# Optimization experiments

Hardware: AMD Instinct MI355X
Metric: run time of the kernel (lower is better)

The kernel has to match this reference:

```python
import jax, jax.numpy as jnp
import numpy as np

L, H, FF, NH = 6, 1024, 4096, 8
HD = H // NH
B, S = 4, 1024
EPS = 1e-5


def _fp8_roundtrip(w):
    # matches torch path: cast to float8_e4m3fn and back (done once at init, no grad)
    return w.astype(jnp.float8_e4m3fn).astype(w.dtype)


def setup_inputs() -> dict:
    key = jax.random.key(0)
    ks = jax.random.split(key, 6)
    x = jax.random.normal(ks[0], (B, S, H), dtype=jnp.float32)
    sH = 1.0 / np.sqrt(H)
    sF = 1.0 / np.sqrt(FF)
    qkv_w = _fp8_roundtrip(jax.random.normal(ks[1], (L, 3 * H, H), jnp.float32) * sH)
    proj_w = _fp8_roundtrip(jax.random.normal(ks[2], (L, H, H), jnp.float32) * sH)
    fc1_w = _fp8_roundtrip(jax.random.normal(ks[3], (L, FF, H), jnp.float32) * sH)
    fc2_w = _fp8_roundtrip(jax.random.normal(ks[4], (L, H, FF), jnp.float32) * sF)
    return {
        "x": x,
        "qkv_w": qkv_w, "qkv_b": jnp.zeros((L, 3 * H), jnp.float32),
        "proj_w": proj_w, "proj_b": jnp.zeros((L, H), jnp.float32),
        "fc1_w": fc1_w, "fc1_b": jnp.zeros((L, FF), jnp.float32),
        "fc2_w": fc2_w, "fc2_b": jnp.zeros((L, H), jnp.float32),
        "ln1_s": jnp.ones((L, H), jnp.float32), "ln1_b": jnp.zeros((L, H), jnp.float32),
        "ln2_s": jnp.ones((L, H), jnp.float32), "ln2_b": jnp.zeros((L, H), jnp.float32),
    }


def _layernorm(x, scale, bias):
    mu = jnp.mean(x, axis=-1, keepdims=True)
    var = jnp.var(x, axis=-1, keepdims=True)
    return (x - mu) / jnp.sqrt(var + EPS) * scale + bias


def reference(x, qkv_w, qkv_b, proj_w, proj_b, fc1_w, fc1_b, fc2_w, fc2_b,
              ln1_s, ln1_b, ln2_s, ln2_b):
    b, s, h = x.shape
    for i in range(L):
        # --- attention block ---
        residual = x
        hx = _layernorm(x, ln1_s[i], ln1_b[i])
        qkv = hx @ qkv_w[i].T + qkv_b[i]                       # [b, s, 3h]
        q, k, v = jnp.split(qkv, 3, axis=-1)
        q = q.reshape(b, s, NH, HD).transpose(0, 2, 1, 3)      # [b, nh, s, hd]
        k = k.reshape(b, s, NH, HD).transpose(0, 2, 1, 3)
        v = v.reshape(b, s, NH, HD).transpose(0, 2, 1, 3)
        scores = jnp.einsum('bhqd,bhkd->bhqk', q, k) / np.sqrt(HD)
        attn = jax.nn.softmax(scores, axis=-1)
        out = jnp.einsum('bhqk,bhkd->bhqd', attn, v)           # [b, nh, s, hd]
        out = out.transpose(0, 2, 1, 3).reshape(b, s, h)
        x = out @ proj_w[i].T + proj_b[i] + residual
        # --- FFN block ---
        residual = x
        hx = _layernorm(x, ln2_s[i], ln2_b[i])
        ff = jax.nn.relu(hx @ fc1_w[i].T + fc1_b[i])
        x = ff @ fc2_w[i].T + fc2_b[i] + residual
    return x
```

## Files before the change

### kernel.cpp

```cpp
#include <hip/hip_runtime.h>
#include <stdint.h>

typedef __bf16 bf16;
typedef __bf16 bf16x4 __attribute__((ext_vector_type(4)));
typedef __bf16 bf16x8 __attribute__((ext_vector_type(8)));
typedef float  f32x4  __attribute__((ext_vector_type(4)));

#define NLAYER 6
#define HDIM   1024
#define FFDIM  4096
#define NHEAD  8
#define HEADD  128
#define SEQ    1024
#define NTOK   4096

__device__ __forceinline__ void g2l16(const void* g, void* l) {
  __builtin_amdgcn_global_load_lds(
      (const __attribute__((address_space(1))) void*)g,
      (__attribute__((address_space(3))) void*)l, 16, 0, 0);
}

__global__ __launch_bounds__(256) void cvt_w(const float* __restrict__ in,
                                             bf16* __restrict__ out, int n8) {
  int i = blockIdx.x * 256 + threadIdx.x;
  if (i >= n8) return;
  const f32x4* p = (const f32x4*)in + (size_t)i * 2;
  f32x4 a = p[0], b = p[1];
  bf16x8 o;
  o[0] = (bf16)a[0]; o[1] = (bf16)a[1]; o[2] = (bf16)a[2]; o[3] = (bf16)a[3];
  o[4] = (bf16)b[0]; o[5] = (bf16)b[1]; o[6] = (bf16)b[2]; o[7] = (bf16)b[3];
  *((bf16x8*)out + i) = o;
}

__global__ __launch_bounds__(256) void ln_k(const float* __restrict__ x,
                                            const float* __restrict__ sc,
                                            const float* __restrict__ bi,
                                            bf16* __restrict__ out) {
  int row = blockIdx.x, t = threadIdx.x;
  f32x4 v = *((const f32x4*)(x + (size_t)row * HDIM) + t);
  float s = v[0] + v[1] + v[2] + v[3];
  float q = v[0]*v[0] + v[1]*v[1] + v[2]*v[2] + v[3]*v[3];
#pragma unroll
  for (int m = 1; m < 64; m <<= 1) {
    s += __shfl_xor(s, m, 64);
    q += __shfl_xor(q, m, 64);
  }
  __shared__ float ss[4], qq[4];
  if ((t & 63) == 0) { ss[t >> 6] = s; qq[t >> 6] = q; }
  __syncthreads();
  s = ss[0] + ss[1] + ss[2] + ss[3];
  q = qq[0] + qq[1] + qq[2] + qq[3];
  float mu  = s * (1.f / HDIM);
  float var = q * (1.f / HDIM) - mu * mu;
  float rs  = rsqrtf(var + 1e-5f);
  f32x4 g = *((const f32x4*)sc + t);
  f32x4 b = *((const f32x4*)bi + t);
  bf16x4 o;
#pragma unroll
  for (int j = 0; j < 4; j++) o[j] = (bf16)((v[j] - mu) * rs * g[j] + b[j]);
  *((bf16x4*)(out + (size_t)row * HDIM) + t) = o;
}

template <bool RELU, bool RESID, bool OUTF32, bool SPLITV>
__global__ __launch_bounds__(256) void gemm_bt(const bf16* __restrict__ A,
                                               const bf16* __restrict__ W,
                                               const float* __restrict__ bias,
                                               const float* resid, void* outp,
                                               bf16* __restrict__ vt,
                                               int M, int N, int K) {
  constexpr int BK = 64;
  __shared__ bf16 As[128 * BK];
  __shared__ bf16 Bs[128 * BK];
  int tid = threadIdx.x;
  int lane = tid & 63, w = tid >> 6;
  int g = lane >> 4, r = lane & 15;
  int wr = w >> 1, wc = w & 1;
  int nbx = N >> 7;
  int bm = blockIdx.x / nbx, bn = blockIdx.x % nbx;
  const bf16* Ab = A + (size_t)bm * 128 * K;
  const bf16* Wb = W + (size_t)bn * 128 * K;
  f32x4 acc[4][4] = {};

  for (int k0 = 0; k0 < K; k0 += BK) {
#pragma unroll
    for (int i = 0; i < 4; ++i) {
      int cb = i * 256 + w * 64;
      int c  = cb + lane;
      int row = c >> 3;
      int kk  = ((c & 7) ^ (row & 7)) << 3;
      g2l16(Ab + (size_t)row * K + k0 + kk, (char*)As + cb * 16);
      g2l16(Wb + (size_t)row * K + k0 + kk, (char*)Bs + cb * 16);
    }
    __syncthreads();
#pragma unroll
    for (int ks = 0; ks < 2; ++ks) {
      bf16x8 af[4], bfr[4];
#pragma unroll
      for (int mi = 0; mi < 4; mi++) {
        int row = wr * 64 + mi * 16 + r;
        af[mi] = *(const bf16x8*)((const char*)As + row * 128 +
                                  ((ks * 64 + g * 16) ^ ((row & 7) << 4)));
      }
#pragma unroll
      for (int ni = 0; ni < 4; ni++) {
        int row = wc * 64 + ni * 16 + r;
        bfr[ni] = *(const bf16x8*)((const char*)Bs + row * 128 +
                                   ((ks * 64 + g * 16) ^ ((row & 7) << 4)));
      }
#pragma unroll
      for (int mi = 0; mi < 4; mi++)
#pragma unroll
        for (int ni = 0; ni < 4; ni++)
          acc[mi][ni] = __builtin_amdgcn_mfma_f32_16x16x32_bf16(
              af[mi], bfr[ni], acc[mi][ni], 0, 0, 0);
    }
    __syncthreads();
  }

#pragma unroll
  for (int ni = 0; ni < 4; ++ni) {
    int col = bn * 128 + wc * 64 + ni * 16 + r;
    float bv = bias[col];
    bool vpart = SPLITV && (bn * 128 + wc * 64 + ni * 16) >= 2048;
    if (vpart) {
      int hh = (col - 2048) >> 7, dd = col & 127;
#pragma unroll
      for (int mi = 0; mi < 4; ++mi) {
        int row0 = bm * 128 + wr * 64 + mi * 16 + g * 4;
        int bb = row0 >> 10, ss = row0 & 1023;
        bf16x4 o;
#pragma unroll
        for (int j = 0; j < 4; j++) o[j] = (bf16)(acc[mi][ni][j] + bv);
        *(bf16x4*)(vt + ((size_t)((bb * NHEAD + hh) * HEADD + dd)) * SEQ + ss) = o;
      }
    } else {
#pragma unroll
      for (int mi = 0; mi < 4; ++mi) {
        int row0 = bm * 128 + wr * 64 + mi * 16 + g * 4;
#pragma unroll
        for (int j = 0; j < 4; j++) {
          size_t idx = (size_t)(row0 + j) * N + col;
          float v = acc[mi][ni][j] + bv;
          if constexpr (RELU) v = fmaxf(v, 0.f);
          if constexpr (RESID) v += resid[idx];
          if constexpr (OUTF32) ((float*)outp)[idx] = v;
          else                  ((bf16*)outp)[idx] = (bf16)v;
        }
      }
    }
  }
}

__global__ __launch_bounds__(256) void attn_k(const bf16* __restrict__ qkv,
                                              const bf16* __restrict__ vt,
                                              bf16* __restrict__ out) {
  __shared__ bf16 Ks[64 * 128];
  __shared__ bf16 VT[128 * 64];
  __shared__ bf16 Ps[4][1024];
  int qt = blockIdx.x, h = blockIdx.y, b = blockIdx.z;
  int tid = threadIdx.x, lane = tid & 63, w = tid >> 6;
  int g = lane >> 4, r = lane & 15;
  int q0 = qt * 64;
  size_t tok0 = (size_t)b * SEQ;
  char* psw = (char*)Ps + w * 2048;

  bf16x8 qf[4];
  {
    const bf16* qp = qkv + (tok0 + q0 + w * 16 + r) * 3072 + h * HEADD;
#pragma unroll
    for (int ks = 0; ks < 4; ks++) qf[ks] = *(const bf16x8*)(qp + ks * 32 + g * 8);
  }
  f32x4 oacc[8] = {};
  float mprev[4], lsum[4];
#pragma unroll
  for (int j = 0; j < 4; j++) { mprev[j] = -1e30f; lsum[j] = 0.f; }
  const float scl = 0.08838834764831845f;
  const bf16* vtb = vt + (size_t)(b * NHEAD + h) * HEADD * SEQ;

  for (int c0 = 0; c0 < SEQ; c0 += 64) {
    const bf16* kbase = qkv + (tok0 + c0) * 3072 + 1024 + h * HEADD;
#pragma unroll
    for (int i = 0; i < 4; i++) {
      int cb = i * 256 + w * 64;
      int c  = cb + lane;
      int krow = c >> 4;
      int kkk  = ((c & 15) ^ (krow & 7)) << 3;
      g2l16(kbase + (size_t)krow * 3072 + kkk, (char*)Ks + cb * 16);
      int vrow = c >> 3;
      int vcol = ((c & 7) ^ (vrow & 7)) << 3;
      g2l16(vtb + (size_t)vrow * SEQ + c0 + vcol, (char*)VT + cb * 16);
    }
    __syncthreads();

    f32x4 sacc[4] = {};
#pragma unroll
    for (int ks = 0; ks < 4; ks++) {
#pragma unroll
      for (int cb = 0; cb < 4; cb++) {
        int row = cb * 16 + r;
        bf16x8 kf = *(const bf16x8*)((const char*)Ks + row * 256 +
                                     ((ks * 64 + g * 16) ^ ((row & 7) << 4)));
        sacc[cb] = __builtin_amdgcn_mfma_f32_16x16x32_bf16(qf[ks], kf, sacc[cb], 0, 0, 0);
      }
    }
#pragma unroll
    for (int cb = 0; cb < 4; cb++) {
      sacc[cb][0] *= scl; sacc[cb][1] *= scl; sacc[cb][2] *= scl; sacc[cb][3] *= scl;
    }
    float sf[4];
#pragma unroll
    for (int j = 0; j < 4; j++) {
      float m = fmaxf(fmaxf(sacc[0][j], sacc[1][j]), fmaxf(sacc[2][j], sacc[3][j]));
      m = fmaxf(m, __shfl_xor(m, 1, 64));
      m = fmaxf(m, __shfl_xor(m, 2, 64));
      m = fmaxf(m, __shfl_xor(m, 4, 64));
      m = fmaxf(m, __shfl_xor(m, 8, 64));
      float mn = fmaxf(mprev[j], m);
      float f  = __expf(mprev[j] - mn);
      mprev[j] = mn; sf[j] = f;
      float rs = 0.f;
#pragma unroll
      for (int cb = 0; cb < 4; cb++) {
        float p = __expf(sacc[cb][j] - mn);
        sacc[cb][j] = p; rs += p;
      }
      rs += __shfl_xor(rs, 1, 64);
      rs += __shfl_xor(rs, 2, 64);
      rs += __shfl_xor(rs, 4, 64);
      rs += __shfl_xor(rs, 8, 64);
      lsum[j] = lsum[j] * f + rs;
    }
#pragma unroll
    for (int nb = 0; nb < 8; nb++) {
      oacc[nb][0] *= sf[0]; oacc[nb][1] *= sf[1];
      oacc[nb][2] *= sf[2]; oacc[nb][3] *= sf[3];
    }
#pragma unroll
    for (int cb = 0; cb < 4; cb++) {
      int cbyte = cb * 32 + r * 2;
#pragma unroll
      for (int j = 0; j < 4; j++) {
        int q = g * 4 + j;
        *(bf16*)(psw + q * 128 + (cbyte ^ ((q & 7) << 4))) = (bf16)sacc[cb][j];
      }
    }
    asm volatile("s_waitcnt lgkmcnt(0)" ::: "memory");
    __builtin_amdgcn_sched_barrier(0);
#pragma unroll
    for (int cs = 0; cs < 2; cs++) {
      bf16x8 pf = *(const bf16x8*)(psw + r * 128 + ((cs * 64 + g * 16) ^ ((r & 7) << 4)));
#pragma unroll
      for (int nb = 0; nb < 8; nb++) {
        int vrow = nb * 16 + r;
        bf16x8 vf = *(const bf16x8*)((const char*)VT + vrow * 128 +
                                     ((cs * 64 + g * 16) ^ ((vrow & 7) << 4)));
        oacc[nb] = __builtin_amdgcn_mfma_f32_16x16x32_bf16(pf, vf, oacc[nb], 0, 0, 0);
      }
    }
    __syncthreads();
  }

  float rl[4];
#pragma unroll
  for (int j = 0; j < 4; j++) rl[j] = 1.f / lsum[j];
#pragma unroll
  for (int nb = 0; nb < 8; nb++)
#pragma unroll
    for (int j = 0; j < 4; j++)
      out[(tok0 + q0 + w * 16 + g * 4 + j) * HDIM + h * HEADD + nb * 16 + r] =
          (bf16)(oacc[nb][j] * rl[j]);
}

extern "C" void kernel_launch(void* const* d_in, const int* in_sizes, int n_in,
                              void* d_out, int out_size, void* d_ws, size_t ws_size,
                              hipStream_t stream) {
  const float* x_in   = (const float*)d_in[0];
  const float* qkv_w  = (const float*)d_in[1];
  const float* qkv_b  = (const float*)d_in[2];
  const float* proj_w = (const float*)d_in[3];
  const float* proj_b = (const float*)d_in[4];
  const float* fc1_w  = (const float*)d_in[5];
  const float* fc1_b  = (const float*)d_in[6];
  const float* fc2_w  = (const float*)d_in[7];
  const float* fc2_b  = (const float*)d_in[8];
  const float* ln1_s  = (const float*)d_in[9];
  const float* ln1_b  = (const float*)d_in[10];
  const float* ln2_s  = (const float*)d_in[11];
  const float* ln2_b  = (const float*)d_in[12];

  char* ws = (char*)d_ws;
  size_t o = 0;
  bf16* Wq = (bf16*)(ws + o); o += (size_t)NLAYER * 3 * HDIM * HDIM * 2;
  bf16* Wp = (bf16*)(ws + o); o += (size_t)NLAYER * HDIM * HDIM * 2;
  bf16* W1 = (bf16*)(ws + o); o += (size_t)NLAYER * FFDIM * HDIM * 2;
  bf16* W2 = (bf16*)(ws + o); o += (size_t)NLAYER * HDIM * FFDIM * 2;
  bf16* hx   = (bf16*)(ws + o); o += (size_t)NTOK * HDIM * 2;
  bf16* qkvb = (bf16*)(ws + o); o += (size_t)NTOK * 3 * HDIM * 2;
  bf16* Vt   = (bf16*)(ws + o); o += (size_t)NTOK * HDIM * 2;
  bf16* aout = (bf16*)(ws + o); o += (size_t)NTOK * HDIM * 2;
  bf16* ffb  = (bf16*)(ws + o); o += (size_t)NTOK * FFDIM * 2;
  float* xbuf = (float*)d_out;

  {
    int n8;
    n8 = NLAYER * 3 * HDIM * HDIM / 8;
    cvt_w<<<(n8 + 255) / 256, 256, 0, stream>>>(qkv_w, Wq, n8);
    n8 = NLAYER * HDIM * HDIM / 8;
    cvt_w<<<(n8 + 255) / 256, 256, 0, stream>>>(proj_w, Wp, n8);
    n8 = NLAYER * FFDIM * HDIM / 8;
    cvt_w<<<(n8 + 255) / 256, 256, 0, stream>>>(fc1_w, W1, n8);
    n8 = NLAYER * HDIM * FFDIM / 8;
    cvt_w<<<(n8 + 255) / 256, 256, 0, stream>>>(fc2_w, W2, n8);
  }

  for (int i = 0; i < NLAYER; i++) {
    const float* xc = (i == 0) ? x_in : xbuf;
    ln_k<<<NTOK, 256, 0, stream>>>(xc, ln1_s + i * HDIM, ln1_b + i * HDIM, hx);
    gemm_bt<false, false, false, true><<<(NTOK / 128) * (3 * HDIM / 128), 256, 0, stream>>>(
        hx, Wq + (size_t)i * 3 * HDIM * HDIM, qkv_b + i * 3 * HDIM, nullptr,
        qkvb, Vt, NTOK, 3 * HDIM, HDIM);
    attn_k<<<dim3(SEQ / 64, NHEAD, 4), 256, 0, stream>>>(qkvb, Vt, aout);
    gemm_bt<false, true, true, false><<<(NTOK / 128) * (HDIM / 128), 256, 0, stream>>>(
        aout, Wp + (size_t)i * HDIM * HDIM, proj_b + i * HDIM, xc,
        xbuf, nullptr, NTOK, HDIM, HDIM);
    ln_k<<<NTOK, 256, 0, stream>>>(xbuf, ln2_s + i * HDIM, ln2_b + i * HDIM, hx);
    gemm_bt<true, false, false, false><<<(NTOK / 128) * (FFDIM / 128), 256, 0, stream>>>(
        hx, W1 + (size_t)i * FFDIM * HDIM, fc1_b + i * FFDIM, nullptr,
        ffb, nullptr, NTOK, FFDIM, HDIM);
    gemm_bt<false, true, true, false><<<(NTOK / 128) * (HDIM / 128), 256, 0, stream>>>(
        ffb, W2 + (size_t)i * HDIM * FFDIM, fc2_b + i * HDIM, xbuf,
        xbuf, nullptr, NTOK, HDIM, FFDIM);
  }
  (void)in_sizes; (void)n_in; (void)out_size; (void)ws_size;
}
```

Measured before the change: 1.761 ms.

## Double-buffer GEMM LDS tiles with 8 waves and XCD-aware block swizzle

```diff
diff --git a/kernel.cpp b/kernel.cpp
--- a/kernel.cpp
+++ b/kernel.cpp
@@ -62,66 +62,80 @@
 }
 
 template <bool RELU, bool RESID, bool OUTF32, bool SPLITV>
-__global__ __launch_bounds__(256) void gemm_bt(const bf16* __restrict__ A,
-                                               const bf16* __restrict__ W,
-                                               const float* __restrict__ bias,
-                                               const float* resid, void* outp,
-                                               bf16* __restrict__ vt,
-                                               int M, int N, int K) {
-  constexpr int BK = 64;
-  __shared__ bf16 As[128 * BK];
-  __shared__ bf16 Bs[128 * BK];
+__global__ __launch_bounds__(512) void gemm8(const bf16* __restrict__ A,
+                                             const bf16* __restrict__ W,
+                                             const float* __restrict__ bias,
+                                             const float* resid, void* outp,
+                                             bf16* __restrict__ vt,
+                                             int M, int N, int K) {
+  __shared__ bf16 As[2][128 * 64];
+  __shared__ bf16 Bs[2][128 * 64];
   int tid = threadIdx.x;
   int lane = tid & 63, w = tid >> 6;
   int g = lane >> 4, r = lane & 15;
-  int wr = w >> 1, wc = w & 1;
+  int wr = w >> 2, wc = w & 3;
   int nbx = N >> 7;
-  int bm = blockIdx.x / nbx, bn = blockIdx.x % nbx;
+  int cpx = gridDim.x >> 3;
+  int swz = (blockIdx.x & 7) * cpx + (blockIdx.x >> 3);
+  int bm = swz / nbx, bn = swz % nbx;
   const bf16* Ab = A + (size_t)bm * 128 * K;
   const bf16* Wb = W + (size_t)bn * 128 * K;
-  f32x4 acc[4][4] = {};
-
-  for (int k0 = 0; k0 < K; k0 += BK) {
-#pragma unroll
-    for (int i = 0; i < 4; ++i) {
-      int cb = i * 256 + w * 64;
-      int c  = cb + lane;
+  f32x4 acc[4][2] = {};
+
+  auto STAGE = [&](int buf, int k0) {
+#pragma unroll
+    for (int i = 0; i < 2; ++i) {
+      int c = i * 512 + tid;
       int row = c >> 3;
-      int kk  = ((c & 7) ^ (row & 7)) << 3;
-      g2l16(Ab + (size_t)row * K + k0 + kk, (char*)As + cb * 16);
-      g2l16(Wb + (size_t)row * K + k0 + kk, (char*)Bs + cb * 16);
-    }
-    __syncthreads();
+      int kk = ((c & 7) ^ (row & 7)) << 3;
+      g2l16(Ab + (size_t)row * K + k0 + kk, (char*)As[buf] + c * 16);
+      g2l16(Wb + (size_t)row * K + k0 + kk, (char*)Bs[buf] + c * 16);
+    }
+  };
+  auto COMPUTE = [&](int buf) {
 #pragma unroll
     for (int ks = 0; ks < 2; ++ks) {
-      bf16x8 af[4], bfr[4];
+      bf16x8 af[4], bfr[2];
 #pragma unroll
       for (int mi = 0; mi < 4; mi++) {
         int row = wr * 64 + mi * 16 + r;
-        af[mi] = *(const bf16x8*)((const char*)As + row * 128 +
+        af[mi] = *(const bf16x8*)((const char*)As[buf] + row * 128 +
                                   ((ks * 64 + g * 16) ^ ((row & 7) << 4)));
       }
 #pragma unroll
-      for (int ni = 0; ni < 4; ni++) {
-        int row = wc * 64 + ni * 16 + r;
-        bfr[ni] = *(const bf16x8*)((const char*)Bs + row * 128 +
+      for (int ni = 0; ni < 2; ni++) {
+        int row = wc * 32 + ni * 16 + r;
+        bfr[ni] = *(const bf16x8*)((const char*)Bs[buf] + row * 128 +
                                    ((ks * 64 + g * 16) ^ ((row & 7) << 4)));
       }
+      __builtin_amdgcn_s_setprio(1);
 #pragma unroll
       for (int mi = 0; mi < 4; mi++)
 #pragma unroll
-        for (int ni = 0; ni < 4; ni++)
+        for (int ni = 0; ni < 2; ni++)
           acc[mi][ni] = __builtin_amdgcn_mfma_f32_16x16x32_bf16(
               af[mi], bfr[ni], acc[mi][ni], 0, 0, 0);
-    }
+      __builtin_amdgcn_s_setprio(0);
+    }
+  };
+
+  int nt = K >> 6;
+  STAGE(0, 0);
+  __syncthreads();
+  int cur = 0;
+  for (int t = 0; t < nt - 1; ++t) {
+    STAGE(cur ^ 1, (t + 1) << 6);
+    COMPUTE(cur);
     __syncthreads();
-  }
-
-#pragma unroll
-  for (int ni = 0; ni < 4; ++ni) {
-    int col = bn * 128 + wc * 64 + ni * 16 + r;
+    cur ^= 1;
+  }
+  COMPUTE(cur);
+
+#pragma unroll
+  for (int ni = 0; ni < 2; ++ni) {
+    int col = bn * 128 + wc * 32 + ni * 16 + r;
     float bv = bias[col];
-    bool vpart = SPLITV && (bn * 128 + wc * 64 + ni * 16) >= 2048;
+    bool vpart = SPLITV && (bn * 128 + wc * 32 + ni * 16) >= 2048;
     if (vpart) {
       int hh = (col - 2048) >> 7, dd = col & 127;
 #pragma unroll
@@ -316,18 +330,18 @@
   for (int i = 0; i < NLAYER; i++) {
     const float* xc = (i == 0) ? x_in : xbuf;
     ln_k<<<NTOK, 256, 0, stream>>>(xc, ln1_s + i * HDIM, ln1_b + i * HDIM, hx);
-    gemm_bt<false, false, false, true><<<(NTOK / 128) * (3 * HDIM / 128), 256, 0, stream>>>(
+    gemm8<false, false, false, true><<<(NTOK / 128) * (3 * HDIM / 128), 512, 0, stream>>>(
         hx, Wq + (size_t)i * 3 * HDIM * HDIM, qkv_b + i * 3 * HDIM, nullptr,
         qkvb, Vt, NTOK, 3 * HDIM, HDIM);
     attn_k<<<dim3(SEQ / 64, NHEAD, 4), 256, 0, stream>>>(qkvb, Vt, aout);
-    gemm_bt<false, true, true, false><<<(NTOK / 128) * (HDIM / 128), 256, 0, stream>>>(
+    gemm8<false, true, true, false><<<(NTOK / 128) * (HDIM / 128), 512, 0, stream>>>(
         aout, Wp + (size_t)i * HDIM * HDIM, proj_b + i * HDIM, xc,
         xbuf, nullptr, NTOK, HDIM, HDIM);
     ln_k<<<NTOK, 256, 0, stream>>>(xbuf, ln2_s + i * HDIM, ln2_b + i * HDIM, hx);
-    gemm_bt<true, false, false, false><<<(NTOK / 128) * (FFDIM / 128), 256, 0, stream>>>(
+    gemm8<true, false, false, false><<<(NTOK / 128) * (FFDIM / 128), 512, 0, stream>>>(
         hx, W1 + (size_t)i * FFDIM * HDIM, fc1_b + i * FFDIM, nullptr,
         ffb, nullptr, NTOK, FFDIM, HDIM);
-    gemm_bt<false, true, true, false><<<(NTOK / 128) * (HDIM / 128), 256, 0, stream>>>(
+    gemm8<false, true, true, false><<<(NTOK / 128) * (HDIM / 128), 512, 0, stream>>>(
         ffb, W2 + (size_t)i * HDIM * FFDIM, fc2_b + i * HDIM, xbuf,
         xbuf, nullptr, NTOK, HDIM, FFDIM);
   }
```

Result: faster. 1.567 ms (-11.0%).

## Add 4-stage LDS prefetch pipeline and XCD block swizzle to GEMM

Applied to the files above, without the earlier changes.

```diff
diff --git a/kernel.cpp b/kernel.cpp
--- a/kernel.cpp
+++ b/kernel.cpp
@@ -62,60 +62,88 @@
 }
 
 template <bool RELU, bool RESID, bool OUTF32, bool SPLITV>
-__global__ __launch_bounds__(256) void gemm_bt(const bf16* __restrict__ A,
-                                               const bf16* __restrict__ W,
-                                               const float* __restrict__ bias,
-                                               const float* resid, void* outp,
-                                               bf16* __restrict__ vt,
-                                               int M, int N, int K) {
-  constexpr int BK = 64;
-  __shared__ bf16 As[128 * BK];
-  __shared__ bf16 Bs[128 * BK];
+__global__ __launch_bounds__(256) void gemm4(const bf16* __restrict__ A,
+                                             const bf16* __restrict__ W,
+                                             const float* __restrict__ bias,
+                                             const float* resid, void* outp,
+                                             bf16* __restrict__ vt,
+                                             int M, int N, int K) {
+  __shared__ bf16 As[4][128 * 64];
+  __shared__ bf16 Bs[4][128 * 64];
   int tid = threadIdx.x;
   int lane = tid & 63, w = tid >> 6;
   int g = lane >> 4, r = lane & 15;
   int wr = w >> 1, wc = w & 1;
   int nbx = N >> 7;
-  int bm = blockIdx.x / nbx, bn = blockIdx.x % nbx;
+  int cpx = gridDim.x >> 3;
+  int swz = (blockIdx.x & 7) * cpx + (blockIdx.x >> 3);
+  int bm = swz / nbx, bn = swz % nbx;
   const bf16* Ab = A + (size_t)bm * 128 * K;
   const bf16* Wb = W + (size_t)bn * 128 * K;
   f32x4 acc[4][4] = {};
 
-  for (int k0 = 0; k0 < K; k0 += BK) {
+  auto STAGE = [&](int buf, int k0) {
 #pragma unroll
     for (int i = 0; i < 4; ++i) {
-      int cb = i * 256 + w * 64;
-      int c  = cb + lane;
+      int c = i * 256 + tid;
       int row = c >> 3;
-      int kk  = ((c & 7) ^ (row & 7)) << 3;
-      g2l16(Ab + (size_t)row * K + k0 + kk, (char*)As + cb * 16);
-      g2l16(Wb + (size_t)row * K + k0 + kk, (char*)Bs + cb * 16);
-    }
-    __syncthreads();
+      int kk = ((c & 7) ^ (row & 7)) << 3;
+      g2l16(Ab + (size_t)row * K + k0 + kk, (char*)As[buf] + c * 16);
+      g2l16(Wb + (size_t)row * K + k0 + kk, (char*)Bs[buf] + c * 16);
+    }
+  };
+  auto COMPUTE = [&](int buf) {
 #pragma unroll
     for (int ks = 0; ks < 2; ++ks) {
       bf16x8 af[4], bfr[4];
 #pragma unroll
       for (int mi = 0; mi < 4; mi++) {
         int row = wr * 64 + mi * 16 + r;
-        af[mi] = *(const bf16x8*)((const char*)As + row * 128 +
+        af[mi] = *(const bf16x8*)((const char*)As[buf] + row * 128 +
                                   ((ks * 64 + g * 16) ^ ((row & 7) << 4)));
       }
 #pragma unroll
       for (int ni = 0; ni < 4; ni++) {
         int row = wc * 64 + ni * 16 + r;
-        bfr[ni] = *(const bf16x8*)((const char*)Bs + row * 128 +
+        bfr[ni] = *(const bf16x8*)((const char*)Bs[buf] + row * 128 +
                                    ((ks * 64 + g * 16) ^ ((row & 7) << 4)));
       }
+      __builtin_amdgcn_s_setprio(1);
 #pragma unroll
       for (int mi = 0; mi < 4; mi++)
 #pragma unroll
         for (int ni = 0; ni < 4; ni++)
           acc[mi][ni] = __builtin_amdgcn_mfma_f32_16x16x32_bf16(
               af[mi], bfr[ni], acc[mi][ni], 0, 0, 0);
-    }
-    __syncthreads();
-  }
+      __builtin_amdgcn_s_setprio(0);
+    }
+  };
+
+  int nt = K >> 6;
+  STAGE(0, 0);
+  STAGE(1, 64);
+  STAGE(2, 128);
+  int t = 0;
+  for (; t < nt - 3; ++t) {
+    asm volatile("s_waitcnt vmcnt(16)" ::: "memory");
+    __builtin_amdgcn_s_barrier();
+    __builtin_amdgcn_sched_barrier(0);
+    STAGE((t + 3) & 3, (t + 3) << 6);
+    __builtin_amdgcn_sched_barrier(0);
+    COMPUTE(t & 3);
+  }
+  asm volatile("s_waitcnt vmcnt(16)" ::: "memory");
+  __builtin_amdgcn_s_barrier();
+  __builtin_amdgcn_sched_barrier(0);
+  COMPUTE(t & 3); ++t;
+  asm volatile("s_waitcnt vmcnt(8)" ::: "memory");
+  __builtin_amdgcn_s_barrier();
+  __builtin_amdgcn_sched_barrier(0);
+  COMPUTE(t & 3); ++t;
+  asm volatile("s_waitcnt vmcnt(0)" ::: "memory");
+  __builtin_amdgcn_s_barrier();
+  __builtin_amdgcn_sched_barrier(0);
+  COMPUTE(t & 3);
 
 #pragma unroll
   for (int ni = 0; ni < 4; ++ni) {
@@ -149,6 +177,7 @@
       }
     }
   }
+  (void)M;
 }
 
 __global__ __launch_bounds__(256) void attn_k(const bf16* __restrict__ qkv,
@@ -316,18 +345,18 @@
   for (int i = 0; i < NLAYER; i++) {
     const float* xc = (i == 0) ? x_in : xbuf;
     ln_k<<<NTOK, 256, 0, stream>>>(xc, ln1_s + i * HDIM, ln1_b + i * HDIM, hx);
-    gemm_bt<false, false, false, true><<<(NTOK / 128) * (3 * HDIM / 128), 256, 0, stream>>>(
+    gemm4<false, false, false, true><<<(NTOK / 128) * (3 * HDIM / 128), 256, 0, stream>>>(
         hx, Wq + (size_t)i * 3 * HDIM * HDIM, qkv_b + i * 3 * HDIM, nullptr,
         qkvb, Vt, NTOK, 3 * HDIM, HDIM);
     attn_k<<<dim3(SEQ / 64, NHEAD, 4), 256, 0, stream>>>(qkvb, Vt, aout);
-    gemm_bt<false, true, true, false><<<(NTOK / 128) * (HDIM / 128), 256, 0, stream>>>(
+    gemm4<false, true, true, false><<<(NTOK / 128) * (HDIM / 128), 256, 0, stream>>>(
         aout, Wp + (size_t)i * HDIM * HDIM, proj_b + i * HDIM, xc,
         xbuf, nullptr, NTOK, HDIM, HDIM);
     ln_k<<<NTOK, 256, 0, stream>>>(xbuf, ln2_s + i * HDIM, ln2_b + i * HDIM, hx);
-    gemm_bt<true, false, false, false><<<(NTOK / 128) * (FFDIM / 128), 256, 0, stream>>>(
+    gemm4<true, false, false, false><<<(NTOK / 128) * (FFDIM / 128), 256, 0, stream>>>(
         hx, W1 + (size_t)i * FFDIM * HDIM, fc1_b + i * FFDIM, nullptr,
         ffb, nullptr, NTOK, FFDIM, HDIM);
-    gemm_bt<false, true, true, false><<<(NTOK / 128) * (HDIM / 128), 256, 0, stream>>>(
+    gemm4<false, true, true, false><<<(NTOK / 128) * (HDIM / 128), 256, 0, stream>>>(
         ffb, W2 + (size_t)i * HDIM * FFDIM, fc2_b + i * HDIM, xbuf,
         xbuf, nullptr, NTOK, HDIM, FFDIM);
   }
```

Result: slower. 1.947 ms (+10.6%).

## Split-K the N=1024 GEMMs with atomic accumulation and swizzle block order

Applied to the files above, without the earlier changes.

```diff
diff --git a/kernel.cpp b/kernel.cpp
--- a/kernel.cpp
+++ b/kernel.cpp
@@ -61,35 +61,49 @@
   *((bf16x4*)(out + (size_t)row * HDIM) + t) = o;
 }
 
-template <bool RELU, bool RESID, bool OUTF32, bool SPLITV>
-__global__ __launch_bounds__(256) void gemm_bt(const bf16* __restrict__ A,
+__global__ __launch_bounds__(256) void init_k(const float* __restrict__ resid,
+                                              const float* __restrict__ bias,
+                                              float* __restrict__ out) {
+  int i = blockIdx.x * 256 + threadIdx.x;
+  f32x4 b = *((const f32x4*)bias + (i & 255));
+  f32x4 v = *((const f32x4*)resid + i);
+  *((f32x4*)out + i) = v + b;
+}
+
+template <int SPLIT, bool RELU, bool RESID, bool OUTF32, bool SPLITV>
+__global__ __launch_bounds__(256) void gemm_sb(const bf16* __restrict__ A,
                                                const bf16* __restrict__ W,
                                                const float* __restrict__ bias,
                                                const float* resid, void* outp,
                                                bf16* __restrict__ vt,
-                                               int M, int N, int K) {
-  constexpr int BK = 64;
-  __shared__ bf16 As[128 * BK];
-  __shared__ bf16 Bs[128 * BK];
+                                               int N, int K) {
+  __shared__ bf16 As[128 * 64];
+  __shared__ bf16 Bs[128 * 64];
   int tid = threadIdx.x;
   int lane = tid & 63, w = tid >> 6;
   int g = lane >> 4, r = lane & 15;
   int wr = w >> 1, wc = w & 1;
   int nbx = N >> 7;
-  int bm = blockIdx.x / nbx, bn = blockIdx.x % nbx;
+  int cpx = gridDim.x >> 3;
+  int swz = (blockIdx.x & 7) * cpx + (blockIdx.x >> 3);
+  int bm = swz / nbx, bn = swz % nbx;
   const bf16* Ab = A + (size_t)bm * 128 * K;
   const bf16* Wb = W + (size_t)bn * 128 * K;
   f32x4 acc[4][4] = {};
 
-  for (int k0 = 0; k0 < K; k0 += BK) {
+  int Ksub = K / SPLIT;
+  int kbase = (SPLIT > 1) ? (int)blockIdx.y * Ksub : 0;
+  int nt = Ksub >> 6;
+
+  for (int t = 0; t < nt; ++t) {
+    int k0 = kbase + (t << 6);
 #pragma unroll
     for (int i = 0; i < 4; ++i) {
-      int cb = i * 256 + w * 64;
-      int c  = cb + lane;
+      int c = i * 256 + tid;
       int row = c >> 3;
-      int kk  = ((c & 7) ^ (row & 7)) << 3;
-      g2l16(Ab + (size_t)row * K + k0 + kk, (char*)As + cb * 16);
-      g2l16(Wb + (size_t)row * K + k0 + kk, (char*)Bs + cb * 16);
+      int kk = ((c & 7) ^ (row & 7)) << 3;
+      g2l16(Ab + (size_t)row * K + k0 + kk, (char*)As + c * 16);
+      g2l16(Wb + (size_t)row * K + k0 + kk, (char*)Bs + c * 16);
     }
     __syncthreads();
 #pragma unroll
@@ -107,44 +121,58 @@
         bfr[ni] = *(const bf16x8*)((const char*)Bs + row * 128 +
                                    ((ks * 64 + g * 16) ^ ((row & 7) << 4)));
       }
+      __builtin_amdgcn_s_setprio(1);
 #pragma unroll
       for (int mi = 0; mi < 4; mi++)
 #pragma unroll
         for (int ni = 0; ni < 4; ni++)
           acc[mi][ni] = __builtin_amdgcn_mfma_f32_16x16x32_bf16(
               af[mi], bfr[ni], acc[mi][ni], 0, 0, 0);
+      __builtin_amdgcn_s_setprio(0);
     }
     __syncthreads();
   }
 
 #pragma unroll
   for (int ni = 0; ni < 4; ++ni) {
-    int col = bn * 128 + wc * 64 + ni * 16 + r;
-    float bv = bias[col];
-    bool vpart = SPLITV && (bn * 128 + wc * 64 + ni * 16) >= 2048;
-    if (vpart) {
-      int hh = (col - 2048) >> 7, dd = col & 127;
+    int cbase = bn * 128 + wc * 64 + ni * 16;
+    int col = cbase + r;
+    if constexpr (SPLIT > 1) {
 #pragma unroll
       for (int mi = 0; mi < 4; ++mi) {
         int row0 = bm * 128 + wr * 64 + mi * 16 + g * 4;
-        int bb = row0 >> 10, ss = row0 & 1023;
-        bf16x4 o;
-#pragma unroll
-        for (int j = 0; j < 4; j++) o[j] = (bf16)(acc[mi][ni][j] + bv);
-        *(bf16x4*)(vt + ((size_t)((bb * NHEAD + hh) * HEADD + dd)) * SEQ + ss) = o;
+#pragma unroll
+        for (int j = 0; j < 4; j++)
+          unsafeAtomicAdd((float*)outp + (size_t)(row0 + j) * N + col,
+                          acc[mi][ni][j]);
       }
     } else {
-#pragma unroll
-      for (int mi = 0; mi < 4; ++mi) {
-        int row0 = bm * 128 + wr * 64 + mi * 16 + g * 4;
-#pragma unroll
-        for (int j = 0; j < 4; j++) {
-          size_t idx = (size_t)(row0 + j) * N + col;
-          float v = acc[mi][ni][j] + bv;
-          if constexpr (RELU) v = fmaxf(v, 0.f);
-          if constexpr (RESID) v += resid[idx];
-          if constexpr (OUTF32) ((float*)outp)[idx] = v;
-          else                  ((bf16*)outp)[idx] = (bf16)v;
+      float bv = bias[col];
+      bool vpart = SPLITV && cbase >= 2048;
+      if (vpart) {
+        int hh = (col - 2048) >> 7, dd = col & 127;
+#pragma unroll
+        for (int mi = 0; mi < 4; ++mi) {
+          int row0 = bm * 128 + wr * 64 + mi * 16 + g * 4;
+          int bb = row0 >> 10, ss = row0 & 1023;
+          bf16x4 o;
+#pragma unroll
+          for (int j = 0; j < 4; j++) o[j] = (bf16)(acc[mi][ni][j] + bv);
+          *(bf16x4*)(vt + ((size_t)((bb * NHEAD + hh) * HEADD + dd)) * SEQ + ss) = o;
+        }
+      } else {
+#pragma unroll
+        for (int mi = 0; mi < 4; ++mi) {
+          int row0 = bm * 128 + wr * 64 + mi * 16 + g * 4;
+#pragma unroll
+          for (int j = 0; j < 4; j++) {
+            size_t idx = (size_t)(row0 + j) * N + col;
+            float v = acc[mi][ni][j] + bv;
+            if constexpr (RELU) v = fmaxf(v, 0.f);
+            if constexpr (RESID) v += resid[idx];
+            if constexpr (OUTF32) ((float*)outp)[idx] = v;
+            else                  ((bf16*)outp)[idx] = (bf16)v;
+          }
         }
       }
     }
@@ -313,23 +341,31 @@
     cvt_w<<<(n8 + 255) / 256, 256, 0, stream>>>(fc2_w, W2, n8);
   }
 
+  const int initg = NTOK * HDIM / 4 / 256;
+
   for (int i = 0; i < NLAYER; i++) {
     const float* xc = (i == 0) ? x_in : xbuf;
     ln_k<<<NTOK, 256, 0, stream>>>(xc, ln1_s + i * HDIM, ln1_b + i * HDIM, hx);
-    gemm_bt<false, false, false, true><<<(NTOK / 128) * (3 * HDIM / 128), 256, 0, stream>>>(
+    gemm_sb<1, false, false, false, true>
+        <<<(NTOK / 128) * (3 * HDIM / 128), 256, 0, stream>>>(
         hx, Wq + (size_t)i * 3 * HDIM * HDIM, qkv_b + i * 3 * HDIM, nullptr,
-        qkvb, Vt, NTOK, 3 * HDIM, HDIM);
+        qkvb, Vt, 3 * HDIM, HDIM);
     attn_k<<<dim3(SEQ / 64, NHEAD, 4), 256, 0, stream>>>(qkvb, Vt, aout);
-    gemm_bt<false, true, true, false><<<(NTOK / 128) * (HDIM / 128), 256, 0, stream>>>(
-        aout, Wp + (size_t)i * HDIM * HDIM, proj_b + i * HDIM, xc,
-        xbuf, nullptr, NTOK, HDIM, HDIM);
+    init_k<<<initg, 256, 0, stream>>>(xc, proj_b + i * HDIM, xbuf);
+    gemm_sb<4, false, false, true, false>
+        <<<dim3((NTOK / 128) * (HDIM / 128), 4), 256, 0, stream>>>(
+        aout, Wp + (size_t)i * HDIM * HDIM, nullptr, nullptr,
+        xbuf, nullptr, HDIM, HDIM);
     ln_k<<<NTOK, 256, 0, stream>>>(xbuf, ln2_s + i * HDIM, ln2_b + i * HDIM, hx);
-    gemm_bt<true, false, false, false><<<(NTOK / 128) * (FFDIM / 128), 256, 0, stream>>>(
+    gemm_sb<1, true, false, false, false>
+        <<<(NTOK / 128) * (FFDIM / 128), 256, 0, stream>>>(
         hx, W1 + (size_t)i * FFDIM * HDIM, fc1_b + i * FFDIM, nullptr,
-        ffb, nullptr, NTOK, FFDIM, HDIM);
-    gemm_bt<false, true, true, false><<<(NTOK / 128) * (HDIM / 128), 256, 0, stream>>>(
-        ffb, W2 + (size_t)i * HDIM * FFDIM, fc2_b + i * HDIM, xbuf,
-        xbuf, nullptr, NTOK, HDIM, FFDIM);
+        ffb, nullptr, FFDIM, HDIM);
+    init_k<<<initg, 256, 0, stream>>>(xbuf, fc2_b + i * HDIM, xbuf);
+    gemm_sb<4, false, false, true, false>
+        <<<dim3((NTOK / 128) * (HDIM / 128), 4), 256, 0, stream>>>(
+        ffb, W2 + (size_t)i * HDIM * FFDIM, nullptr, nullptr,
+        xbuf, nullptr, HDIM, FFDIM);
   }
   (void)in_sizes; (void)n_in; (void)out_size; (void)ws_size;
 }
```

After: 1.858 ms. 5.5% more time.
